# Performance work log

Hardware: AMD Instinct MI355X
Metric: run time of the kernel (lower is better)

Reference implementation:

```python
import jax, jax.numpy as jnp
import numpy as np

IN_CH = 128
N_HEAD = 16
D_K = 4
D_MODEL = 256
T_PE = 1000.0
EPS = 1e-5


def setup_inputs() -> dict:
    key = jax.random.key(0)
    ks = jax.random.split(key, 8)
    sz_b, L, h, w = 4, 30, 64, 64
    x = jax.random.normal(ks[0], (sz_b, L, IN_CH, h, w), dtype=jnp.float32)
    batch_positions = jnp.sort(jax.random.randint(ks[1], (sz_b, L), 0, 365), axis=1).astype(jnp.int32)
    pad_mask = jnp.zeros((sz_b, L), dtype=bool)
    gn_weight = jnp.ones((IN_CH,), dtype=jnp.float32)
    gn_bias = jnp.zeros((IN_CH,), dtype=jnp.float32)
    conv_w = jax.random.normal(ks[2], (D_MODEL, IN_CH), dtype=jnp.float32) * (1.0 / np.sqrt(IN_CH))
    conv_b = jnp.zeros((D_MODEL,), dtype=jnp.float32)
    Q = jax.random.normal(ks[3], (N_HEAD, D_K), dtype=jnp.float32) * np.sqrt(2.0 / D_K)
    Wk = jax.random.normal(ks[4], (N_HEAD * D_K, D_MODEL), dtype=jnp.float32) * np.sqrt(2.0 / D_K)
    bk = jnp.zeros((N_HEAD * D_K,), dtype=jnp.float32)
    return {"x": x, "gn_weight": gn_weight, "gn_bias": gn_bias,
            "conv_w": conv_w, "conv_b": conv_b, "Q": Q, "Wk": Wk, "bk": bk,
            "batch_positions": batch_positions, "pad_mask": pad_mask}


def reference(x, gn_weight, gn_bias, conv_w, conv_b, Q, Wk, bk, batch_positions, pad_mask):
    n_head, d_k = Q.shape
    sz_b, L, d, h, w = x.shape
    B = sz_b * h * w
    # flatten pixels: [B, L, C]
    out = x.transpose(0, 3, 4, 1, 2).reshape(B, L, d)
    # GroupNorm(num_groups=n_head) over channels and time per pixel-sample
    g = out.transpose(0, 2, 1).reshape(B, n_head, d // n_head, L)
    mu = g.mean(axis=(2, 3), keepdims=True)
    var = g.var(axis=(2, 3), keepdims=True)
    g = (g - mu) / jnp.sqrt(var + EPS)
    out = g.reshape(B, d, L) * gn_weight[None, :, None] + gn_bias[None, :, None]
    out = out.transpose(0, 2, 1)  # [B, L, C]
    # 1x1 Conv1d == per-timestep linear projection to d_model
    out = out @ conv_w.T + conv_b  # [B, L, d_model]
    d_model = conv_w.shape[0]
    # sinusoidal positional encoding on dates, repeated over heads
    d_pe = d_model // n_head
    idx = jnp.arange(d_pe)
    denom = jnp.power(jnp.float32(T_PE), 2.0 * (idx // 2).astype(jnp.float32) / d_pe)
    tab = batch_positions.astype(jnp.float32)[:, :, None] / denom  # [sz_b, L, d_pe]
    pe = jnp.where(idx % 2 == 0, jnp.sin(tab), jnp.cos(tab))
    pe = jnp.tile(pe, (1, 1, n_head))  # [sz_b, L, d_model]
    out = (out.reshape(sz_b, h * w, L, d_model) + pe[:, None, :, :]).reshape(B, L, d_model)
    # keys and learned-query attention scores, temperature = sqrt(d_k)
    k = (out @ Wk.T + bk).reshape(B, L, n_head, d_k)
    scores = jnp.einsum('hd,blhd->hbl', Q, k) / jnp.sqrt(jnp.float32(d_k))
    scores = scores.reshape(n_head, sz_b, h * w, L)
    scores = jnp.where(pad_mask[None, :, None, :], jnp.float32(-1000.0), scores)
    attn = jax.nn.softmax(scores, axis=-1)
    # [n_head, sz_b, L, h, w]
    return attn.reshape(n_head, sz_b, h, w, L).transpose(0, 1, 4, 2, 3)
```

## Files before the change

### kernel.cpp

```cpp
#include <hip/hip_runtime.h>


#define SZB  4
#define LLEN 30
#define INC  128
#define NH   16
#define HW   4096
#define NPIX 16384
#define EPSV 1e-5f

#define WS_U    0
#define WS_UU   2048
#define WS_P2   2304
#define WS_FLAG 4224
#define WS_QT   4352
#define WS_WT   8448
#define WS_INV  10496
#define WS_MUI  272640

__global__ void k0a(const float* __restrict__ Q, const float* __restrict__ Wk,
                    float* __restrict__ ws) {
    int h = blockIdx.x, m = threadIdx.x;
    float s = 0.f;
    #pragma unroll
    for (int d = 0; d < 4; ++d) s += Q[h*4+d] * Wk[(h*4+d)*256 + m];
    ws[WS_QT + h*256 + m] = s;
}

__global__ void k0b(const float* __restrict__ conv_w, const float* __restrict__ gn_w,
                    float* __restrict__ ws) {
    int idx = blockIdx.x*256 + threadIdx.x;
    int h = idx >> 7, c = idx & 127;
    const float* qt = ws + WS_QT + h*256;
    float s = 0.f;
    #pragma unroll 8
    for (int m = 0; m < 256; ++m) s += qt[m] * conv_w[m*128 + c];
    ws[WS_WT + h*128 + c] = s;
    ws[WS_U  + c*16  + h] = s * gn_w[c];
}

__global__ void k0c(const float* __restrict__ Q, const float* __restrict__ conv_b,
                    const float* __restrict__ gn_b, const float* __restrict__ bk,
                    const int* __restrict__ bpos, const unsigned char* __restrict__ pmask,
                    float* __restrict__ ws) {
    __shared__ float sc[16];
    __shared__ float qsv[256];
    __shared__ float rden[16];
    int t = threadIdx.x;
    {
        int h = t >> 4, g = t & 15;
        float s = 0.f;
        #pragma unroll
        for (int cc = 0; cc < 8; ++cc) s += ws[WS_U + (g*8+cc)*16 + h];
        ws[WS_UU + g*16 + h] = s;
    }
    {
        int h = t >> 4, p = t & 15;
        float s = 0.f;
        #pragma unroll
        for (int r = 0; r < 16; ++r) s += ws[WS_QT + h*256 + r*16 + p];
        qsv[h*16 + p] = s;
    }
    if (t < 16) {
        int h = t;
        float wb = 0.f;
        for (int c = 0; c < 128; ++c) wb += ws[WS_WT + h*128 + c] * gn_b[c];
        float s0 = 0.f;
        for (int m = 0; m < 256; ++m) s0 += ws[WS_QT + h*256 + m] * conv_b[m];
        #pragma unroll
        for (int d = 0; d < 4; ++d) s0 += Q[h*4+d] * bk[h*4+d];
        sc[h] = wb + s0;
        rden[t] = powf(1000.0f, -((float)(t >> 1)) * 0.125f);
    }
    if (t < 120) ws[WS_FLAG + t] = pmask[t] ? 1.f : 0.f;
    __syncthreads();
    for (int idx = t; idx < 1920; idx += 256) {
        int h = idx / 120, r = idx % 120;
        float pos = (float)bpos[r];
        float pt = 0.f;
        #pragma unroll
        for (int p = 0; p < 16; ++p) {
            float tab = pos * rden[p];
            float v = (p & 1) ? cosf(tab) : sinf(tab);
            pt += v * qsv[h*16 + p];
        }
        ws[WS_P2 + r*16 + h] = pt + sc[h];
    }
}

__global__ void __launch_bounds__(256) k1(const float* __restrict__ x,
                                          float* __restrict__ ws) {
    int bx = blockIdx.x;
    int g = bx >> 6, pb = bx & 63;
    int pix = pb*256 + threadIdx.x;
    int b = pix >> 12, pij = pix & 4095;
    const float* xp = x + (b*30*128 + g*8)*4096 + pij;
    float s = 0.f, ss = 0.f;
    for (int l = 0; l < 30; ++l) {
        const float* xl = xp + l*128*4096;
        #pragma unroll
        for (int c = 0; c < 8; ++c) {
            float v = xl[c*4096];
            s += v; ss += v*v;
        }
    }
    float mu  = s * (1.f/240.f);
    float var = ss * (1.f/240.f) - mu*mu;
    float inv = rsqrtf(var + EPSV);
    ws[WS_INV + g*16384 + pix] = inv;
    ws[WS_MUI + g*16384 + pix] = mu * inv;
}

__global__ void __launch_bounds__(256) k2(const float* __restrict__ x,
                                          const float* __restrict__ ws,
                                          float* __restrict__ out) {
    __shared__ float su[2048];
    __shared__ float sU[256];
    __shared__ float sP2[16];
    __shared__ float sflag;
    int t = threadIdx.x;
    int bx = blockIdx.x;
    int pb = bx / 30, l = bx % 30;
    int pix = pb*256 + t;
    int b = pix >> 12, pij = pix & 4095;
    int bl = b*30 + l;
    for (int i = t; i < 2048; i += 256) su[i] = ws[WS_U + i];
    sU[t] = ws[WS_UU + t];
    if (t < 16) sP2[t] = ws[WS_P2 + bl*16 + t];
    if (t == 0) sflag = ws[WS_FLAG + bl];
    __syncthreads();

    float acc[16];
    #pragma unroll
    for (int h = 0; h < 16; ++h) acc[h] = 0.f;
    const float* xbase = x + (bl*128)*4096 + pij;
    for (int g = 0; g < 16; ++g) {
        float inv = ws[WS_INV + g*16384 + pix];
        float mui = ws[WS_MUI + g*16384 + pix];
        const float* us = su + g*8*16;
        const float* Ug = sU + g*16;
        #pragma unroll
        for (int h = 0; h < 16; ++h) acc[h] -= mui * Ug[h];
        const float* xg = xbase + g*8*4096;
        #pragma unroll
        for (int cc = 0; cc < 8; ++cc) {
            float xs = xg[cc*4096] * inv;
            #pragma unroll
            for (int h = 0; h < 16; ++h) acc[h] += us[cc*16 + h] * xs;
        }
    }
    bool msk = (sflag != 0.f);
    #pragma unroll
    for (int h = 0; h < 16; ++h) {
        float sv = 0.5f * (acc[h] + sP2[h]);
        if (msk) sv = -1000.f;
        out[((h*4 + b)*30 + l)*4096 + pij] = sv;
    }
}

__global__ void __launch_bounds__(256) k3(float* __restrict__ out) {
    int idx = blockIdx.x*256 + threadIdx.x;
    int hb = idx >> 12, pij = idx & 4095;
    float* p = out + hb*30*4096 + pij;
    float v[30];
    float m = -1e30f;
    #pragma unroll
    for (int l = 0; l < 30; ++l) { v[l] = p[l*4096]; m = fmaxf(m, v[l]); }
    float s = 0.f;
    #pragma unroll
    for (int l = 0; l < 30; ++l) { v[l] = __expf(v[l] - m); s += v[l]; }
    float r = 1.f / s;
    #pragma unroll
    for (int l = 0; l < 30; ++l) p[l*4096] = v[l] * r;
}

extern "C" void kernel_launch(void* const* d_in, const int* in_sizes, int n_in,
                              void* d_out, int out_size, void* d_ws, size_t ws_size,
                              hipStream_t stream) {
    const float* x      = (const float*)d_in[0];
    const float* gn_w   = (const float*)d_in[1];
    const float* gn_b   = (const float*)d_in[2];
    const float* conv_w = (const float*)d_in[3];
    const float* conv_b = (const float*)d_in[4];
    const float* Q      = (const float*)d_in[5];
    const float* Wk     = (const float*)d_in[6];
    const float* bk     = (const float*)d_in[7];
    const int*   bpos   = (const int*)d_in[8];
    const unsigned char* pmask = (const unsigned char*)d_in[9];
    float* ws  = (float*)d_ws;
    float* out = (float*)d_out;

    hipLaunchKernelGGL(k0a, dim3(16),   dim3(256), 0, stream, Q, Wk, ws);
    hipLaunchKernelGGL(k0b, dim3(8),    dim3(256), 0, stream, conv_w, gn_w, ws);
    hipLaunchKernelGGL(k0c, dim3(1),    dim3(256), 0, stream, Q, conv_b, gn_b, bk, bpos, pmask, ws);
    hipLaunchKernelGGL(k1,  dim3(1024), dim3(256), 0, stream, x, ws);
    hipLaunchKernelGGL(k2,  dim3(1920), dim3(256), 0, stream, x, ws, out);
    hipLaunchKernelGGL(k3,  dim3(1024), dim3(256), 0, stream, out);
}
```

Baseline: 163.5 us.

## Merge setup kernels into one block and process two pixels per thread with float2

Merges the three small weight-precompute kernels into a single 1024-thread block kernel with __syncthreads between phases, cutting two launches. The stats, projection and softmax kernels now handle two adjacent pixels per thread using float2 loads and stores, which halves the grid sizes and doubles the register accumulators in k2. The aim is wider memory transactions and less per-launch overhead. The cost is fewer blocks, higher register pressure in k2 and a serial single-block setup phase.

Result: no change. 163.1 us (-0.2%).

```diff
diff --git a/kernel.cpp b/kernel.cpp
--- a/kernel.cpp
+++ b/kernel.cpp
@@ -1,12 +1,6 @@
 #include <hip/hip_runtime.h>
 
 
-#define SZB  4
-#define LLEN 30
-#define INC  128
-#define NH   16
-#define HW   4096
-#define NPIX 16384
 #define EPSV 1e-5f
 
 #define WS_U    0
@@ -18,48 +12,48 @@
 #define WS_INV  10496
 #define WS_MUI  272640
 
-__global__ void k0a(const float* __restrict__ Q, const float* __restrict__ Wk,
-                    float* __restrict__ ws) {
-    int h = blockIdx.x, m = threadIdx.x;
-    float s = 0.f;
-    #pragma unroll
-    for (int d = 0; d < 4; ++d) s += Q[h*4+d] * Wk[(h*4+d)*256 + m];
-    ws[WS_QT + h*256 + m] = s;
-}
-
-__global__ void k0b(const float* __restrict__ conv_w, const float* __restrict__ gn_w,
-                    float* __restrict__ ws) {
-    int idx = blockIdx.x*256 + threadIdx.x;
-    int h = idx >> 7, c = idx & 127;
-    const float* qt = ws + WS_QT + h*256;
-    float s = 0.f;
-    #pragma unroll 8
-    for (int m = 0; m < 256; ++m) s += qt[m] * conv_w[m*128 + c];
-    ws[WS_WT + h*128 + c] = s;
-    ws[WS_U  + c*16  + h] = s * gn_w[c];
-}
-
-__global__ void k0c(const float* __restrict__ Q, const float* __restrict__ conv_b,
-                    const float* __restrict__ gn_b, const float* __restrict__ bk,
-                    const int* __restrict__ bpos, const unsigned char* __restrict__ pmask,
-                    float* __restrict__ ws) {
+__global__ void __launch_bounds__(1024) k0(const float* __restrict__ Q,
+                                           const float* __restrict__ Wk,
+                                           const float* __restrict__ conv_w,
+                                           const float* __restrict__ gn_w,
+                                           const float* __restrict__ conv_b,
+                                           const float* __restrict__ gn_b,
+                                           const float* __restrict__ bk,
+                                           const int* __restrict__ bpos,
+                                           const unsigned char* __restrict__ pmask,
+                                           float* __restrict__ ws) {
+    int t = threadIdx.x;
+    for (int i = t; i < 4096; i += 1024) {
+        int h = i >> 8, m = i & 255;
+        float s = 0.f;
+        #pragma unroll
+        for (int d = 0; d < 4; ++d) s += Q[h*4+d] * Wk[(h*4+d)*256 + m];
+        ws[WS_QT + h*256 + m] = s;
+    }
+    __syncthreads();
+    for (int i = t; i < 2048; i += 1024) {
+        int h = i >> 7, c = i & 127;
+        const float* qt = ws + WS_QT + h*256;
+        float s = 0.f;
+        #pragma unroll 8
+        for (int m = 0; m < 256; ++m) s += qt[m] * conv_w[m*128 + c];
+        ws[WS_WT + h*128 + c] = s;
+        ws[WS_U  + c*16  + h] = s * gn_w[c];
+    }
+    __syncthreads();
     __shared__ float sc[16];
     __shared__ float qsv[256];
     __shared__ float rden[16];
-    int t = threadIdx.x;
-    {
+    if (t < 256) {
         int h = t >> 4, g = t & 15;
         float s = 0.f;
         #pragma unroll
         for (int cc = 0; cc < 8; ++cc) s += ws[WS_U + (g*8+cc)*16 + h];
         ws[WS_UU + g*16 + h] = s;
-    }
-    {
-        int h = t >> 4, p = t & 15;
-        float s = 0.f;
-        #pragma unroll
-        for (int r = 0; r < 16; ++r) s += ws[WS_QT + h*256 + r*16 + p];
-        qsv[h*16 + p] = s;
+        float q = 0.f;
+        #pragma unroll
+        for (int r = 0; r < 16; ++r) q += ws[WS_QT + h*256 + r*16 + g];
+        qsv[h*16 + g] = q;
     }
     if (t < 16) {
         int h = t;
@@ -74,8 +68,8 @@
     }
     if (t < 120) ws[WS_FLAG + t] = pmask[t] ? 1.f : 0.f;
     __syncthreads();
-    for (int idx = t; idx < 1920; idx += 256) {
-        int h = idx / 120, r = idx % 120;
+    for (int idx = t; idx < 1920; idx += 1024) {
+        int h = idx / 120, r = idx - h*120;
         float pos = (float)bpos[r];
         float pt = 0.f;
         #pragma unroll
@@ -91,24 +85,26 @@
 __global__ void __launch_bounds__(256) k1(const float* __restrict__ x,
                                           float* __restrict__ ws) {
     int bx = blockIdx.x;
-    int g = bx >> 6, pb = bx & 63;
-    int pix = pb*256 + threadIdx.x;
-    int b = pix >> 12, pij = pix & 4095;
-    const float* xp = x + (b*30*128 + g*8)*4096 + pij;
-    float s = 0.f, ss = 0.f;
-    for (int l = 0; l < 30; ++l) {
-        const float* xl = xp + l*128*4096;
+    int g = bx >> 5;
+    int pq = (bx & 31)*256 + threadIdx.x;
+    int pix0 = pq*2;
+    int b = pix0 >> 12, pij = pix0 & 4095;
+    const float2* xp = (const float2*)(x + (b*30*128 + g*8)*4096 + pij);
+    float sx = 0.f, sy = 0.f, ssx = 0.f, ssy = 0.f;
+    for (int l = 0; l < 30; ++l) {
+        const float2* xl = xp + l*128*2048;
         #pragma unroll
         for (int c = 0; c < 8; ++c) {
-            float v = xl[c*4096];
-            s += v; ss += v*v;
+            float2 v = xl[c*2048];
+            sx += v.x; sy += v.y;
+            ssx += v.x*v.x; ssy += v.y*v.y;
         }
     }
-    float mu  = s * (1.f/240.f);
-    float var = ss * (1.f/240.f) - mu*mu;
-    float inv = rsqrtf(var + EPSV);
-    ws[WS_INV + g*16384 + pix] = inv;
-    ws[WS_MUI + g*16384 + pix] = mu * inv;
+    float mux = sx*(1.f/240.f), muy = sy*(1.f/240.f);
+    float ivx = rsqrtf(ssx*(1.f/240.f) - mux*mux + EPSV);
+    float ivy = rsqrtf(ssy*(1.f/240.f) - muy*muy + EPSV);
+    *(float2*)(ws + WS_INV + g*16384 + pix0) = make_float2(ivx, ivy);
+    *(float2*)(ws + WS_MUI + g*16384 + pix0) = make_float2(mux*ivx, muy*ivy);
 }
 
 __global__ void __launch_bounds__(256) k2(const float* __restrict__ x,
@@ -120,9 +116,9 @@
     __shared__ float sflag;
     int t = threadIdx.x;
     int bx = blockIdx.x;
-    int pb = bx / 30, l = bx % 30;
-    int pix = pb*256 + t;
-    int b = pix >> 12, pij = pix & 4095;
+    int pb2 = bx / 30, l = bx - pb2*30;
+    int pix0 = (pb2*256 + t)*2;
+    int b = pix0 >> 12, pij = pix0 & 4095;
     int bl = b*30 + l;
     for (int i = t; i < 2048; i += 256) su[i] = ws[WS_U + i];
     sU[t] = ws[WS_UU + t];
@@ -130,48 +126,62 @@
     if (t == 0) sflag = ws[WS_FLAG + bl];
     __syncthreads();
 
-    float acc[16];
-    #pragma unroll
-    for (int h = 0; h < 16; ++h) acc[h] = 0.f;
+    float a0[16], a1[16];
+    #pragma unroll
+    for (int h = 0; h < 16; ++h) { a0[h] = 0.f; a1[h] = 0.f; }
     const float* xbase = x + (bl*128)*4096 + pij;
     for (int g = 0; g < 16; ++g) {
-        float inv = ws[WS_INV + g*16384 + pix];
-        float mui = ws[WS_MUI + g*16384 + pix];
-        const float* us = su + g*8*16;
+        float2 inv = *(const float2*)(ws + WS_INV + g*16384 + pix0);
+        float2 mui = *(const float2*)(ws + WS_MUI + g*16384 + pix0);
+        const float* us = su + g*128;
         const float* Ug = sU + g*16;
         #pragma unroll
-        for (int h = 0; h < 16; ++h) acc[h] -= mui * Ug[h];
+        for (int h = 0; h < 16; ++h) { a0[h] -= mui.x*Ug[h]; a1[h] -= mui.y*Ug[h]; }
         const float* xg = xbase + g*8*4096;
         #pragma unroll
         for (int cc = 0; cc < 8; ++cc) {
-            float xs = xg[cc*4096] * inv;
+            float2 v = *(const float2*)(xg + cc*4096);
+            float xs0 = v.x*inv.x, xs1 = v.y*inv.y;
             #pragma unroll
-            for (int h = 0; h < 16; ++h) acc[h] += us[cc*16 + h] * xs;
+            for (int h = 0; h < 16; ++h) {
+                float uu = us[cc*16 + h];
+                a0[h] += uu*xs0; a1[h] += uu*xs1;
+            }
         }
     }
     bool msk = (sflag != 0.f);
     #pragma unroll
     for (int h = 0; h < 16; ++h) {
-        float sv = 0.5f * (acc[h] + sP2[h]);
-        if (msk) sv = -1000.f;
-        out[((h*4 + b)*30 + l)*4096 + pij] = sv;
+        float s0 = 0.5f*(a0[h] + sP2[h]);
+        float s1 = 0.5f*(a1[h] + sP2[h]);
+        if (msk) { s0 = -1000.f; s1 = -1000.f; }
+        *(float2*)(out + ((h*4 + b)*30 + l)*4096 + pij) = make_float2(s0, s1);
     }
 }
 
 __global__ void __launch_bounds__(256) k3(float* __restrict__ out) {
     int idx = blockIdx.x*256 + threadIdx.x;
-    int hb = idx >> 12, pij = idx & 4095;
+    int hb = idx >> 11;
+    int pij = (idx & 2047)*2;
     float* p = out + hb*30*4096 + pij;
-    float v[30];
-    float m = -1e30f;
-    #pragma unroll
-    for (int l = 0; l < 30; ++l) { v[l] = p[l*4096]; m = fmaxf(m, v[l]); }
-    float s = 0.f;
-    #pragma unroll
-    for (int l = 0; l < 30; ++l) { v[l] = __expf(v[l] - m); s += v[l]; }
-    float r = 1.f / s;
-    #pragma unroll
-    for (int l = 0; l < 30; ++l) p[l*4096] = v[l] * r;
+    float2 v[30];
+    float m0 = -1e30f, m1 = -1e30f;
+    #pragma unroll
+    for (int l = 0; l < 30; ++l) {
+        v[l] = *(const float2*)(p + l*4096);
+        m0 = fmaxf(m0, v[l].x); m1 = fmaxf(m1, v[l].y);
+    }
+    float s0 = 0.f, s1 = 0.f;
+    #pragma unroll
+    for (int l = 0; l < 30; ++l) {
+        v[l].x = __expf(v[l].x - m0); s0 += v[l].x;
+        v[l].y = __expf(v[l].y - m1); s1 += v[l].y;
+    }
+    float r0 = 1.f/s0, r1 = 1.f/s1;
+    #pragma unroll
+    for (int l = 0; l < 30; ++l) {
+        *(float2*)(p + l*4096) = make_float2(v[l].x*r0, v[l].y*r1);
+    }
 }
 
 extern "C" void kernel_launch(void* const* d_in, const int* in_sizes, int n_in,
@@ -190,10 +200,9 @@
     float* ws  = (float*)d_ws;
     float* out = (float*)d_out;
 
-    hipLaunchKernelGGL(k0a, dim3(16),   dim3(256), 0, stream, Q, Wk, ws);
-    hipLaunchKernelGGL(k0b, dim3(8),    dim3(256), 0, stream, conv_w, gn_w, ws);
-    hipLaunchKernelGGL(k0c, dim3(1),    dim3(256), 0, stream, Q, conv_b, gn_b, bk, bpos, pmask, ws);
-    hipLaunchKernelGGL(k1,  dim3(1024), dim3(256), 0, stream, x, ws);
-    hipLaunchKernelGGL(k2,  dim3(1920), dim3(256), 0, stream, x, ws, out);
-    hipLaunchKernelGGL(k3,  dim3(1024), dim3(256), 0, stream, out);
-}
+    hipLaunchKernelGGL(k0, dim3(1),    dim3(1024), 0, stream,
+                       Q, Wk, conv_w, gn_w, conv_b, gn_b, bk, bpos, pmask, ws);
+    hipLaunchKernelGGL(k1, dim3(512),  dim3(256),  0, stream, x, ws);
+    hipLaunchKernelGGL(k2, dim3(960),  dim3(256),  0, stream, x, ws, out);
+    hipLaunchKernelGGL(k3, dim3(512),  dim3(256),  0, stream, out);
+}
```
